# Kernel tuning notes

Hardware: AMD Instinct MI355X
Metric: run time of the kernel (lower is better)

Reference implementation:

```python
import jax, jax.numpy as jnp
import numpy as np


def _unfold_valid(x, kh, kw, stride):
    """torch.nn.Unfold equivalent (valid padding): [B,C,H,W] -> [B, C*kh*kw, L].
    Channel-major patch layout (c, kh, kw), matching PyTorch."""
    B, C, H, W = x.shape
    oh = (H - kh) // stride + 1
    ow = (W - kw) // stride + 1
    i = (jnp.arange(oh) * stride)[:, None] + jnp.arange(kh)  # [oh, kh]
    j = (jnp.arange(ow) * stride)[:, None] + jnp.arange(kw)  # [ow, kw]
    # advanced indexing broadcasts to [B, C, oh, ow, kh, kw]
    p = x[:, :, i[:, None, :, None], j[None, :, None, :]]
    p = p.transpose(0, 1, 4, 5, 2, 3).reshape(B, C * kh * kw, oh * ow)
    return p


def setup_inputs() -> dict:
    root = jax.random.key(0)
    k1, k2 = jax.random.split(root)
    query = jax.random.normal(k1, (4, 32, 64, 64), dtype=jnp.float32)
    key = jax.random.normal(k2, (4, 32, 64, 192), dtype=jnp.float32)
    return {"query": query, "key": key}


def reference(query, key):
    stride = 1
    B, C, Hq, Wq = query.shape
    P = key.shape[3] - Wq + 1
    patches = _unfold_valid(key, Hq, Wq, stride)          # [B, D, L], D = C*Hq*Wq
    q = query.reshape(B, C * Hq * Wq, 1)                  # [B, D, 1]
    y = jnp.mean(jnp.abs(patches - q), axis=1)            # [B, L] L1 cost volume
    relevance_maps = jnp.min(y, axis=1, keepdims=True)    # [B, 1]
    hard_indices = jnp.argmin(y, axis=1).reshape(-1)      # [B]
    return hard_indices, P, relevance_maps
```

## Files before the change

kernel.cpp:

```cpp
#include <hip/hip_runtime.h>
#include <math.h>

#define B 4
#define C 32
#define H 64
#define WQ 64
#define WK 192
#define NP 129
#define ROWS (C * H)
#define ELEMS (ROWS * WQ)
#define GB 256
#define WPB 4
#define RPW (ROWS / (GB * WPB))
#define PSTRIDE 132

__global__ __launch_bounds__(256, 4) void patch_l1_partial(const float* __restrict__ query,
                                                           const float* __restrict__ key,
                                                           float* __restrict__ part) {
    __shared__ __align__(16) float kbuf[WPB][RPW * WK];
    __shared__ float red[WPB][NP];

    const int bid  = blockIdx.x;
    const int b    = bid >> 8;
    const int g    = bid & (GB - 1);
    const int t    = threadIdx.x;
    const int wv   = t >> 6;
    const int lane = t & 63;
    const int slot = __builtin_amdgcn_readfirstlane(g * WPB + (t >> 6));
    const int r0   = slot * RPW;

    const float* __restrict__ qb = query + (size_t)b * ELEMS;
    const float* __restrict__ kb = key   + (size_t)b * ROWS * WK + (size_t)r0 * WK;

    if (lane < 48) {
        const float4 k0 = *reinterpret_cast<const float4*>(kb + lane * 4);
        const float4 k1 = *reinterpret_cast<const float4*>(kb + WK + lane * 4);
        *reinterpret_cast<float4*>(&kbuf[wv][lane * 4])      = k0;
        *reinterpret_cast<float4*>(&kbuf[wv][WK + lane * 4]) = k1;
    }
    const float q0l = qb[(size_t)r0 * WQ + lane];
    const float q1l = qb[(size_t)(r0 + 1) * WQ + lane];

    const float* __restrict__ q0 = qb + (size_t)r0 * WQ;
    const float* __restrict__ q1 = qb + (size_t)(r0 + 1) * WQ;
    const float* __restrict__ k0 = &kbuf[wv][0];
    const float* __restrict__ k1 = &kbuf[wv][WK];

    float a0 = 0.f, b0 = 0.f, a1 = 0.f, b1 = 0.f, acc2 = 0.f;

    #pragma unroll
    for (int si = 0; si < 33; ++si) {
        const int s = si * 2;
        const float2 ka = *reinterpret_cast<const float2*>(&k0[2 * lane + s]);
        const float2 kc = *reinterpret_cast<const float2*>(&k1[2 * lane + s]);
        if (si < 32) {
            a0 += fabsf(ka.x - q0[s]) + fabsf(ka.y - q0[s + 1]);
            a1 += fabsf(kc.x - q1[s]) + fabsf(kc.y - q1[s + 1]);
            b0 += fabsf(ka.y - q0[s]);
            b1 += fabsf(kc.y - q1[s]);
            if (si > 0) {
                b0 += fabsf(ka.x - q0[s - 1]);
                b1 += fabsf(kc.x - q1[s - 1]);
            }
        } else {
            b0 += fabsf(ka.x - q0[63]);
            b1 += fabsf(kc.x - q1[63]);
        }
    }
    acc2 += fabsf(k0[128 + lane] - q0l);
    acc2 += fabsf(k1[128 + lane] - q1l);

    #pragma unroll
    for (int m = 32; m; m >>= 1) acc2 += __shfl_xor(acc2, m, 64);

    red[wv][2 * lane]     = a0 + a1;
    red[wv][2 * lane + 1] = b0 + b1;
    if (lane == 0) red[wv][128] = acc2;
    __syncthreads();

    if (t < NP)
        part[(size_t)bid * PSTRIDE + t] = red[0][t] + red[1][t] + red[2][t] + red[3][t];
}

__global__ __launch_bounds__(256) void patch_l1_final(const float* __restrict__ part,
                                                      float* __restrict__ out) {
    const int b = blockIdx.x;
    const int t = threadIdx.x;

    float y = INFINITY;
    int idx = NP;
    if (t < NP) {
        const float* __restrict__ p0 = part + (size_t)b * GB * PSTRIDE + t;
        float s0 = 0.f, s1 = 0.f, s2 = 0.f, s3 = 0.f;
        #pragma unroll 4
        for (int g = 0; g < GB; g += 4) {
            s0 += p0[(g + 0) * PSTRIDE];
            s1 += p0[(g + 1) * PSTRIDE];
            s2 += p0[(g + 2) * PSTRIDE];
            s3 += p0[(g + 3) * PSTRIDE];
        }
        y = ((s0 + s1) + (s2 + s3)) * (1.0f / (float)ELEMS);
        idx = t;
    }

    __shared__ float sy[256];
    __shared__ int   si[256];
    sy[t] = y;
    si[t] = idx;
    __syncthreads();
    #pragma unroll
    for (int s = 128; s > 0; s >>= 1) {
        if (t < s) {
            const float yo = sy[t + s];
            const int   io = si[t + s];
            if (yo < sy[t] || (yo == sy[t] && io < si[t])) {
                sy[t] = yo;
                si[t] = io;
            }
        }
        __syncthreads();
    }

    if (t == 0) {
        out[b]     = (float)si[0];
        out[5 + b] = sy[0];
        if (b == 0) out[4] = (float)NP;
    }
}

extern "C" void kernel_launch(void* const* d_in, const int* in_sizes, int n_in,
                              void* d_out, int out_size, void* d_ws, size_t ws_size,
                              hipStream_t stream) {
    const float* query = (const float*)d_in[0];
    const float* key   = (const float*)d_in[1];
    float* out  = (float*)d_out;
    float* part = (float*)d_ws;

    patch_l1_partial<<<B * GB, 256, 0, stream>>>(query, key, part);
    patch_l1_final<<<B, 256, 0, stream>>>(part, out);
}
```

Before: 19.98 us.

## Stage query rows in LDS and transpose partials for coalesced final reduction

```diff
diff --git a/kernel.cpp b/kernel.cpp
--- a/kernel.cpp
+++ b/kernel.cpp
@@ -11,13 +11,13 @@
 #define ELEMS (ROWS * WQ)
 #define GB 256
 #define WPB 4
-#define RPW (ROWS / (GB * WPB))
-#define PSTRIDE 132
+#define RPW 2
 
 __global__ __launch_bounds__(256, 4) void patch_l1_partial(const float* __restrict__ query,
                                                            const float* __restrict__ key,
                                                            float* __restrict__ part) {
     __shared__ __align__(16) float kbuf[WPB][RPW * WK];
+    __shared__ __align__(16) float qbuf[WPB][RPW * WQ];
     __shared__ float red[WPB][NP];
 
     const int bid  = blockIdx.x;
@@ -29,24 +29,29 @@
     const int slot = __builtin_amdgcn_readfirstlane(g * WPB + (t >> 6));
     const int r0   = slot * RPW;
 
-    const float* __restrict__ qb = query + (size_t)b * ELEMS;
     const float* __restrict__ kb = key   + (size_t)b * ROWS * WK + (size_t)r0 * WK;
+    const float* __restrict__ qg = query + (size_t)b * ELEMS     + (size_t)r0 * WQ;
 
     if (lane < 48) {
-        const float4 k0 = *reinterpret_cast<const float4*>(kb + lane * 4);
-        const float4 k1 = *reinterpret_cast<const float4*>(kb + WK + lane * 4);
-        *reinterpret_cast<float4*>(&kbuf[wv][lane * 4])      = k0;
-        *reinterpret_cast<float4*>(&kbuf[wv][WK + lane * 4]) = k1;
+        const float4 v0 = *reinterpret_cast<const float4*>(kb + lane * 4);
+        const float4 v1 = *reinterpret_cast<const float4*>(kb + WK + lane * 4);
+        *reinterpret_cast<float4*>(&kbuf[wv][lane * 4])      = v0;
+        *reinterpret_cast<float4*>(&kbuf[wv][WK + lane * 4]) = v1;
+    } else {
+        const int i = lane - 48;
+        const float4 v0 = *reinterpret_cast<const float4*>(qg + i * 4);
+        const float4 v1 = *reinterpret_cast<const float4*>(qg + WQ + i * 4);
+        *reinterpret_cast<float4*>(&qbuf[wv][i * 4])      = v0;
+        *reinterpret_cast<float4*>(&qbuf[wv][WQ + i * 4]) = v1;
     }
-    const float q0l = qb[(size_t)r0 * WQ + lane];
-    const float q1l = qb[(size_t)(r0 + 1) * WQ + lane];
 
-    const float* __restrict__ q0 = qb + (size_t)r0 * WQ;
-    const float* __restrict__ q1 = qb + (size_t)(r0 + 1) * WQ;
     const float* __restrict__ k0 = &kbuf[wv][0];
     const float* __restrict__ k1 = &kbuf[wv][WK];
+    const float* __restrict__ q0 = &qbuf[wv][0];
+    const float* __restrict__ q1 = &qbuf[wv][WQ];
 
-    float a0 = 0.f, b0 = 0.f, a1 = 0.f, b1 = 0.f, acc2 = 0.f;
+    float a0 = 0.f, b0 = 0.f, a1 = 0.f, b1 = 0.f;
+    float pq0 = 0.f, pq1 = 0.f;
 
     #pragma unroll
     for (int si = 0; si < 33; ++si) {
@@ -54,22 +59,25 @@
         const float2 ka = *reinterpret_cast<const float2*>(&k0[2 * lane + s]);
         const float2 kc = *reinterpret_cast<const float2*>(&k1[2 * lane + s]);
         if (si < 32) {
-            a0 += fabsf(ka.x - q0[s]) + fabsf(ka.y - q0[s + 1]);
-            a1 += fabsf(kc.x - q1[s]) + fabsf(kc.y - q1[s + 1]);
-            b0 += fabsf(ka.y - q0[s]);
-            b1 += fabsf(kc.y - q1[s]);
+            const float2 qa = *reinterpret_cast<const float2*>(&q0[s]);
+            const float2 qc = *reinterpret_cast<const float2*>(&q1[s]);
+            a0 += fabsf(ka.x - qa.x) + fabsf(ka.y - qa.y);
+            a1 += fabsf(kc.x - qc.x) + fabsf(kc.y - qc.y);
+            b0 += fabsf(ka.y - qa.x);
+            b1 += fabsf(kc.y - qc.x);
             if (si > 0) {
-                b0 += fabsf(ka.x - q0[s - 1]);
-                b1 += fabsf(kc.x - q1[s - 1]);
+                b0 += fabsf(ka.x - pq0);
+                b1 += fabsf(kc.x - pq1);
             }
+            pq0 = qa.y;
+            pq1 = qc.y;
         } else {
-            b0 += fabsf(ka.x - q0[63]);
-            b1 += fabsf(kc.x - q1[63]);
+            b0 += fabsf(ka.x - pq0);
+            b1 += fabsf(kc.x - pq1);
         }
     }
-    acc2 += fabsf(k0[128 + lane] - q0l);
-    acc2 += fabsf(k1[128 + lane] - q1l);
 
+    float acc2 = fabsf(k0[128 + lane] - q0[lane]) + fabsf(k1[128 + lane] - q1[lane]);
     #pragma unroll
     for (int m = 32; m; m >>= 1) acc2 += __shfl_xor(acc2, m, 64);
 
@@ -78,52 +86,47 @@
     if (lane == 0) red[wv][128] = acc2;
     __syncthreads();
 
-    if (t < NP)
-        part[(size_t)bid * PSTRIDE + t] = red[0][t] + red[1][t] + red[2][t] + red[3][t];
+    if (t < NP) {
+        const float v = red[0][t] + red[1][t] + red[2][t] + red[3][t];
+        part[((size_t)b * NP + t) * GB + g] = v;
+    }
 }
 
 __global__ __launch_bounds__(256) void patch_l1_final(const float* __restrict__ part,
                                                       float* __restrict__ out) {
-    const int b = blockIdx.x;
-    const int t = threadIdx.x;
+    const int b    = blockIdx.x;
+    const int t    = threadIdx.x;
+    const int wv   = t >> 6;
+    const int lane = t & 63;
 
-    float y = INFINITY;
-    int idx = NP;
-    if (t < NP) {
-        const float* __restrict__ p0 = part + (size_t)b * GB * PSTRIDE + t;
-        float s0 = 0.f, s1 = 0.f, s2 = 0.f, s3 = 0.f;
-        #pragma unroll 4
-        for (int g = 0; g < GB; g += 4) {
-            s0 += p0[(g + 0) * PSTRIDE];
-            s1 += p0[(g + 1) * PSTRIDE];
-            s2 += p0[(g + 2) * PSTRIDE];
-            s3 += p0[(g + 3) * PSTRIDE];
-        }
-        y = ((s0 + s1) + (s2 + s3)) * (1.0f / (float)ELEMS);
-        idx = t;
+    float best = INFINITY;
+    int   besti = NP;
+
+    for (int p = wv; p < NP; p += 4) {
+        const float* __restrict__ src = part + ((size_t)b * NP + p) * GB;
+        float v = src[lane] + src[lane + 64] + src[lane + 128] + src[lane + 192];
+        #pragma unroll
+        for (int m = 32; m; m >>= 1) v += __shfl_xor(v, m, 64);
+        const float y = v * (1.0f / (float)ELEMS);
+        if (y < best) { best = y; besti = p; }
     }
 
-    __shared__ float sy[256];
-    __shared__ int   si[256];
-    sy[t] = y;
-    si[t] = idx;
+    __shared__ float sy[4];
+    __shared__ int   si[4];
+    if (lane == 0) { sy[wv] = best; si[wv] = besti; }
     __syncthreads();
-    #pragma unroll
-    for (int s = 128; s > 0; s >>= 1) {
-        if (t < s) {
-            const float yo = sy[t + s];
-            const int   io = si[t + s];
-            if (yo < sy[t] || (yo == sy[t] && io < si[t])) {
-                sy[t] = yo;
-                si[t] = io;
-            }
-        }
-        __syncthreads();
-    }
 
     if (t == 0) {
-        out[b]     = (float)si[0];
-        out[5 + b] = sy[0];
+        float yb = sy[0];
+        int   ib = si[0];
+        #pragma unroll
+        for (int w = 1; w < 4; ++w) {
+            const float yo = sy[w];
+            const int   io = si[w];
+            if (yo < yb || (yo == yb && io < ib)) { yb = yo; ib = io; }
+        }
+        out[b]     = (float)ib;
+        out[5 + b] = yb;
         if (b == 0) out[4] = (float)NP;
     }
 }
```

Measured after the change: 27.66 us. 1.38x slower.

## Fuse final reduction into partial kernel via atomics and last-block argmin

Applied to the files above, without the earlier changes.

```diff
diff --git a/kernel.cpp b/kernel.cpp
--- a/kernel.cpp
+++ b/kernel.cpp
@@ -12,13 +12,16 @@
 #define GB 256
 #define WPB 4
 #define RPW (ROWS / (GB * WPB))
-#define PSTRIDE 132
+#define TOTAL (B * GB)
 
-__global__ __launch_bounds__(256, 4) void patch_l1_partial(const float* __restrict__ query,
-                                                           const float* __restrict__ key,
-                                                           float* __restrict__ part) {
+__global__ __launch_bounds__(256, 4) void patch_l1_fused(const float* __restrict__ query,
+                                                          const float* __restrict__ key,
+                                                          float* __restrict__ sums,
+                                                          unsigned int* __restrict__ counter,
+                                                          float* __restrict__ out) {
     __shared__ __align__(16) float kbuf[WPB][RPW * WK];
     __shared__ float red[WPB][NP];
+    __shared__ int   is_last;
 
     const int bid  = blockIdx.x;
     const int b    = bid >> 8;
@@ -33,10 +36,10 @@
     const float* __restrict__ kb = key   + (size_t)b * ROWS * WK + (size_t)r0 * WK;
 
     if (lane < 48) {
-        const float4 k0 = *reinterpret_cast<const float4*>(kb + lane * 4);
-        const float4 k1 = *reinterpret_cast<const float4*>(kb + WK + lane * 4);
-        *reinterpret_cast<float4*>(&kbuf[wv][lane * 4])      = k0;
-        *reinterpret_cast<float4*>(&kbuf[wv][WK + lane * 4]) = k1;
+        const float4 k0v = *reinterpret_cast<const float4*>(kb + lane * 4);
+        const float4 k1v = *reinterpret_cast<const float4*>(kb + WK + lane * 4);
+        *reinterpret_cast<float4*>(&kbuf[wv][lane * 4])      = k0v;
+        *reinterpret_cast<float4*>(&kbuf[wv][WK + lane * 4]) = k1v;
     }
     const float q0l = qb[(size_t)r0 * WQ + lane];
     const float q1l = qb[(size_t)(r0 + 1) * WQ + lane];
@@ -69,7 +72,6 @@
     }
     acc2 += fabsf(k0[128 + lane] - q0l);
     acc2 += fabsf(k1[128 + lane] - q1l);
-
     #pragma unroll
     for (int m = 32; m; m >>= 1) acc2 += __shfl_xor(acc2, m, 64);
 
@@ -78,53 +80,44 @@
     if (lane == 0) red[wv][128] = acc2;
     __syncthreads();
 
-    if (t < NP)
-        part[(size_t)bid * PSTRIDE + t] = red[0][t] + red[1][t] + red[2][t] + red[3][t];
-}
-
-__global__ __launch_bounds__(256) void patch_l1_final(const float* __restrict__ part,
-                                                      float* __restrict__ out) {
-    const int b = blockIdx.x;
-    const int t = threadIdx.x;
-
-    float y = INFINITY;
-    int idx = NP;
     if (t < NP) {
-        const float* __restrict__ p0 = part + (size_t)b * GB * PSTRIDE + t;
-        float s0 = 0.f, s1 = 0.f, s2 = 0.f, s3 = 0.f;
-        #pragma unroll 4
-        for (int g = 0; g < GB; g += 4) {
-            s0 += p0[(g + 0) * PSTRIDE];
-            s1 += p0[(g + 1) * PSTRIDE];
-            s2 += p0[(g + 2) * PSTRIDE];
-            s3 += p0[(g + 3) * PSTRIDE];
-        }
-        y = ((s0 + s1) + (s2 + s3)) * (1.0f / (float)ELEMS);
-        idx = t;
+        const float v = red[0][t] + red[1][t] + red[2][t] + red[3][t];
+        atomicAdd(&sums[b * NP + t], v);
     }
 
-    __shared__ float sy[256];
-    __shared__ int   si[256];
-    sy[t] = y;
-    si[t] = idx;
+    __threadfence();
+    if (t == 0) {
+        const unsigned int old = atomicAdd(counter, 1u);
+        is_last = (old == TOTAL - 1u) ? 1 : 0;
+    }
     __syncthreads();
-    #pragma unroll
-    for (int s = 128; s > 0; s >>= 1) {
-        if (t < s) {
-            const float yo = sy[t + s];
-            const int   io = si[t + s];
-            if (yo < sy[t] || (yo == sy[t] && io < si[t])) {
-                sy[t] = yo;
-                si[t] = io;
-            }
-        }
-        __syncthreads();
+    if (!is_last) return;
+
+    __threadfence();
+    const volatile float* __restrict__ vs = (const volatile float*)(sums + wv * NP);
+    const float inv = 1.0f / (float)ELEMS;
+
+    const float y0 = vs[lane] * inv;
+    const float y1 = vs[64 + lane] * inv;
+    float best  = y0;
+    int   besti = lane;
+    if (y1 < best) { best = y1; besti = 64 + lane; }
+    if (lane == 0) {
+        const float y2 = vs[128] * inv;
+        if (y2 < best) { best = y2; besti = 128; }
     }
 
-    if (t == 0) {
-        out[b]     = (float)si[0];
-        out[5 + b] = sy[0];
-        if (b == 0) out[4] = (float)NP;
+    #pragma unroll
+    for (int m = 32; m; m >>= 1) {
+        const float yo = __shfl_xor(best, m, 64);
+        const int   io = __shfl_xor(besti, m, 64);
+        if (yo < best || (yo == best && io < besti)) { best = yo; besti = io; }
+    }
+
+    if (lane == 0) {
+        out[wv]     = (float)besti;
+        out[5 + wv] = best;
+        if (wv == 0) out[4] = (float)NP;
     }
 }
 
@@ -134,8 +127,9 @@
     const float* query = (const float*)d_in[0];
     const float* key   = (const float*)d_in[1];
     float* out  = (float*)d_out;
-    float* part = (float*)d_ws;
+    float* sums = (float*)d_ws;
+    unsigned int* counter = (unsigned int*)(sums + B * NP);
 
-    patch_l1_partial<<<B * GB, 256, 0, stream>>>(query, key, part);
-    patch_l1_final<<<B, 256, 0, stream>>>(part, out);
+    hipMemsetAsync(d_ws, 0, (B * NP + 1) * sizeof(float), stream);
+    patch_l1_fused<<<TOTAL, 256, 0, stream>>>(query, key, sums, counter, out);
 }
```

After: 76.58 us. 3.83x slower.
